# Performance work log

Hardware: AMD Instinct MI355X
Metric: run time of the kernel (lower is better)

## Reference

```python
import jax, jax.numpy as jnp
import numpy as np

B, T, D, H = 128, 512, 256, 256


def setup_inputs() -> dict:
    key = jax.random.key(0)
    k1, k2, k3, k4 = jax.random.split(key, 4)
    x = jax.random.normal(k1, (B, T, D), dtype=jnp.float32)
    x_len = jax.random.randint(k2, (B,), 1, T + 1)  # lengths in [1, T]
    W_ih = jax.random.normal(k3, (4 * H, D), dtype=jnp.float32) * 0.05
    W_hh = jax.random.normal(k4, (4 * H, H), dtype=jnp.float32) * 0.05
    b_ih = jnp.zeros((4 * H,), dtype=jnp.float32)
    # reset_params: bias_hh forget-gate chunk (index 1 of i,f,g,o) set to 1
    b_hh = jnp.zeros((4 * H,), dtype=jnp.float32).at[H:2 * H].set(1.0)
    return {"x": x, "x_len": x_len, "W_ih": W_ih, "W_hh": W_hh,
            "b_ih": b_ih, "b_hh": b_hh}


def reference(x, x_len, W_ih, W_hh, b_ih, b_hh):
    # Dropout is identity in eval mode. The sort/pack/unpack pipeline is
    # mathematically equivalent to running a masked LSTM over the padded
    # batch and zeroing outputs at positions t >= x_len (pad_packed_sequence
    # zero-pads), since output at t < len only depends on steps <= t.
    Bx, Tx, _ = x.shape
    Hh = W_hh.shape[1]
    # Precompute input projections for all timesteps: [B, T, 4H] -> [T, B, 4H]
    xg = jnp.einsum('btd,gd->btg', x, W_ih) + b_ih + b_hh
    xg = jnp.swapaxes(xg, 0, 1)

    def step(carry, xt):
        h, c = carry
        gates = xt + h @ W_hh.T  # [B, 4H]
        i, f, g, o = jnp.split(gates, 4, axis=-1)
        i = jax.nn.sigmoid(i)
        f = jax.nn.sigmoid(f)
        g = jnp.tanh(g)
        o = jax.nn.sigmoid(o)
        c = f * c + i * g
        h = o * jnp.tanh(c)
        return (h, c), h

    h0 = jnp.zeros((Bx, Hh), x.dtype)
    (_, _), hs = jax.lax.scan(step, (h0, h0), xg)  # hs: [T, B, H]
    out = jnp.swapaxes(hs, 0, 1)  # [B, T, H]
    mask = jnp.arange(Tx)[None, :] < x_len[:, None]  # [B, T]
    return jnp.where(mask[..., None], out, jnp.zeros((), x.dtype))
```

## Files before the change

kernel.cpp:

```cpp
#include <hip/hip_runtime.h>
#include <hip/hip_fp16.h>
#include <math.h>

#define BB 128
#define TT 512
#define DD 256
#define HH 256
#define NG 1024

typedef _Float16 h2_t __attribute__((ext_vector_type(2)));
typedef _Float16 f16x8 __attribute__((ext_vector_type(8)));
typedef float f32x4 __attribute__((ext_vector_type(4)));

#if __has_builtin(__builtin_amdgcn_fdot2)
__device__ __forceinline__ float fdot2_(h2_t a, h2_t b, float c) {
    return __builtin_amdgcn_fdot2(a, b, c, false);
}
#else
__device__ __forceinline__ float fdot2_(h2_t a, h2_t b, float c) {
    return c + (float)a.x * (float)b.x + (float)a.y * (float)b.y;
}
#endif

__device__ __forceinline__ float sigmoidf_(float x) {
    return 1.0f / (1.0f + __expf(-x));
}
__device__ __forceinline__ float tanhf_(float x) {
    x = fminf(15.0f, fmaxf(-15.0f, x));
    float e = __expf(2.0f * x);
    return (e - 1.0f) / (e + 1.0f);
}
__device__ __forceinline__ void dot4_(float4& acc, uint4 u, h2_t h) {
    acc.x = fdot2_(__builtin_bit_cast(h2_t, u.x), h, acc.x);
    acc.y = fdot2_(__builtin_bit_cast(h2_t, u.y), h, acc.y);
    acc.z = fdot2_(__builtin_bit_cast(h2_t, u.z), h, acc.z);
    acc.w = fdot2_(__builtin_bit_cast(h2_t, u.w), h, acc.w);
}

#if __has_builtin(__builtin_amdgcn_update_dpp)
__device__ __forceinline__ float pair_sum_(float v) {
    int x = __builtin_bit_cast(int, v);
    int y = __builtin_amdgcn_update_dpp(0, x, 0xB1, 0xF, 0xF, true);
    return v + __builtin_bit_cast(float, y);
}
#else
__device__ __forceinline__ float pair_sum_(float v) {
    return v + __shfl_xor(v, 1, 64);
}
#endif

__global__ void pack2(const float* __restrict__ W_ih, const float* __restrict__ W_hh,
                      const float* __restrict__ b_ih, const float* __restrict__ b_hh,
                      __half* __restrict__ Wg16, __half* __restrict__ Wi16,
                      __half* __restrict__ Wh16, float* __restrict__ bias_p) {
    int idx = blockIdx.x * 256 + threadIdx.x;
    int n = idx >> 8;
    int k = idx & 255;
    int g = (n & 3) * 256 + (n >> 2);
    float wih = W_ih[g * 256 + k];
    float whh = W_hh[g * 256 + k];
    Wg16[n * 256 + k] = __float2half(wih);
    size_t hidx = ((size_t)(k >> 1) * 1024 + n) * 2 + (k & 1);
    Wi16[hidx] = __float2half(wih);
    Wh16[hidx] = __float2half(whh);
    if (idx < 1024) {
        int gg = (idx & 3) * 256 + (idx >> 2);
        bias_p[idx] = b_ih[gg] + b_hh[gg];
    }
}

__global__ __launch_bounds__(256) void cvt_x(const float* __restrict__ X,
                                             __half* __restrict__ X16) {
    size_t i = ((size_t)blockIdx.x * 256 + threadIdx.x) * 8;
    float4 a = *(const float4*)&X[i];
    float4 b = *(const float4*)&X[i + 4];
    f16x8 v;
    v[0] = (_Float16)a.x; v[1] = (_Float16)a.y; v[2] = (_Float16)a.z; v[3] = (_Float16)a.w;
    v[4] = (_Float16)b.x; v[5] = (_Float16)b.y; v[6] = (_Float16)b.z; v[7] = (_Float16)b.w;
    *(f16x8*)&X16[i] = v;
}

__global__ __launch_bounds__(256) void xg_gemm_mfma(const __half* __restrict__ X16,
                                                    const __half* __restrict__ Wg16,
                                                    const float* __restrict__ bias_p,
                                                    __half* __restrict__ xg,
                                                    int t0, int lTc, int tcMask) {
    __shared__ __align__(16) __half st[4][16][72];
    int tid = threadIdx.x;
    int w = tid >> 6, lane = tid & 63;
    int row16 = lane & 15, quad = lane >> 4;
    int m0 = blockIdx.x * 64 + w * 16;
    int n0 = blockIdx.y * 64;

    int mrow = m0 + row16;
    size_t xrow = (size_t)(mrow >> lTc) * 512 + t0 + (mrow & tcMask);
    const __half* aptr = X16 + xrow * 256 + quad * 8;
    f16x8 afrag[8];
#pragma unroll
    for (int kk = 0; kk < 8; ++kk)
        afrag[kk] = *(const f16x8*)(aptr + kk * 32);

#pragma unroll
    for (int cg = 0; cg < 4; ++cg) {
        int n = n0 + cg * 16 + row16;
        const __half* bptr = Wg16 + (size_t)n * 256 + quad * 8;
        f32x4 acc = {0.0f, 0.0f, 0.0f, 0.0f};
#pragma unroll
        for (int kk = 0; kk < 8; ++kk) {
            f16x8 bfrag = *(const f16x8*)(bptr + kk * 32);
            acc = __builtin_amdgcn_mfma_f32_16x16x32_f16(afrag[kk], bfrag, acc, 0, 0, 0);
        }
        float bias = bias_p[n];
#pragma unroll
        for (int r = 0; r < 4; ++r)
            st[w][quad * 4 + r][cg * 16 + row16] = __float2half(acc[r] + bias);
    }
    __syncthreads();
    int ml = lane >> 2, cq = lane & 3;
    int mout = blockIdx.x * 64 + w * 16 + ml;
    const uint4* src = (const uint4*)&st[w][ml][cq * 16];
    uint4 v0 = src[0], v1 = src[1];
    *(uint4*)&xg[(size_t)mout * 1024 + n0 + cq * 16] = v0;
    *(uint4*)&xg[(size_t)mout * 1024 + n0 + cq * 16 + 8] = v1;
}

__global__ __launch_bounds__(512, 2) void lstm_rec4(const __half* __restrict__ xg,
                                                    const __half* __restrict__ Wh16,
                                                    const int* __restrict__ x_len,
                                                    float* __restrict__ out,
                                                    __half* __restrict__ h_state,
                                                    float* __restrict__ c_state,
                                                    int t0, int Tc) {
    __shared__ __align__(16) uint4 lw[9728];
    __shared__ __align__(16) __half hs[2][272];
    int tid = threadIdx.x;
    int c = tid >> 1, kh = tid & 1;
    int b = blockIdx.x;
    int len = x_len[b];
    const uint4* W4 = (const uint4*)Wh16;

    for (int j = tid; j < 9728; j += 512) {
        int i2 = j >> 9, c2 = (j >> 1) & 255, kh2 = j & 1;
        lw[j] = W4[(size_t)(kh2 * 64 + 44 + i2) * 256 + c2];
    }
    const uint4* wp = W4 + (size_t)(kh * 64) * 256 + c;
    uint4 wreg[44];
#pragma unroll
    for (int i = 0; i < 44; ++i) wreg[i] = wp[(size_t)i * 256];

    float cst = 0.0f;
    float hlast = 0.0f;
    if (t0 != 0) cst = c_state[b * 256 + c];
    if (kh == 0)
        hs[0][c + ((c >> 7) << 4)] = (t0 == 0) ? __float2half(0.0f)
                                               : h_state[b * 256 + c];

    const __half* xgb = xg + (size_t)b * Tc * 1024 + 4 * c;
    float* outb = out + ((size_t)b * 512 + t0) * 256 + c;
    const uint4* lwb = lw + tid;
    __syncthreads();

    for (int tt = 0; tt < Tc; ++tt) {
        uint4 s0 = wp[(size_t)63 * 256];
        uint2 xr = *(const uint2*)(xgb + (size_t)tt * 1024);

        const uint4* h4 = (const uint4*)(hs[tt & 1]) + kh * 18;
        float4 acc = {0.0f, 0.0f, 0.0f, 0.0f};
#pragma unroll
        for (int j = 0; j < 11; ++j) {
            uint4 hv = h4[j];
            dot4_(acc, wreg[j * 4 + 0], __builtin_bit_cast(h2_t, hv.x));
            dot4_(acc, wreg[j * 4 + 1], __builtin_bit_cast(h2_t, hv.y));
            dot4_(acc, wreg[j * 4 + 2], __builtin_bit_cast(h2_t, hv.z));
            dot4_(acc, wreg[j * 4 + 3], __builtin_bit_cast(h2_t, hv.w));
        }
#pragma unroll
        for (int j = 11; j < 15; ++j) {
            uint4 hv = h4[j];
            int i0 = (j - 11) * 4;
            dot4_(acc, lwb[(i0 + 0) * 512], __builtin_bit_cast(h2_t, hv.x));
            dot4_(acc, lwb[(i0 + 1) * 512], __builtin_bit_cast(h2_t, hv.y));
            dot4_(acc, lwb[(i0 + 2) * 512], __builtin_bit_cast(h2_t, hv.z));
            dot4_(acc, lwb[(i0 + 3) * 512], __builtin_bit_cast(h2_t, hv.w));
        }
        {
            uint4 hv = h4[15];
            dot4_(acc, lwb[16 * 512], __builtin_bit_cast(h2_t, hv.x));
            dot4_(acc, lwb[17 * 512], __builtin_bit_cast(h2_t, hv.y));
            dot4_(acc, lwb[18 * 512], __builtin_bit_cast(h2_t, hv.z));
            dot4_(acc, s0, __builtin_bit_cast(h2_t, hv.w));
        }
        float gi = pair_sum_(acc.x);
        float gf = pair_sum_(acc.y);
        float gg = pair_sum_(acc.z);
        float go = pair_sum_(acc.w);
        h2_t x01 = __builtin_bit_cast(h2_t, xr.x);
        h2_t x23 = __builtin_bit_cast(h2_t, xr.y);
        gi += (float)x01.x;
        gf += (float)x01.y;
        gg += (float)x23.x;
        go += (float)x23.y;
        float iv = sigmoidf_(gi), fv = sigmoidf_(gf);
        float gv = tanhf_(gg),   ov = sigmoidf_(go);
        cst = fv * cst + iv * gv;
        float h = ov * tanhf_(cst);
        hlast = h;
        if (kh == 0) {
            outb[(size_t)tt * 256] = (t0 + tt < len) ? h : 0.0f;
            hs[(tt & 1) ^ 1][c + ((c >> 7) << 4)] = __float2half(h);
        }
        __syncthreads();
    }
    if (kh == 0) {
        h_state[b * 256 + c] = __float2half(hlast);
        c_state[b * 256 + c] = cst;
    }
}

__global__ __launch_bounds__(1024) void lstm_fused16(const float* __restrict__ X,
                                                     const __half* __restrict__ Wi16,
                                                     const __half* __restrict__ Wh16,
                                                     const float* __restrict__ bias_p,
                                                     const int* __restrict__ x_len,
                                                     float* __restrict__ out) {
    __shared__ __half hs_h[256];
    __shared__ __half xs_h[256];
    __shared__ float4 part[3][256];
    int tid = threadIdx.x;
    int c = tid & 255, kh = tid >> 8;
    int b = blockIdx.x;
    int len = x_len[b];
    float cst = 0.0f;
    float4 bias;
    if (kh == 0) {
        bias = *(const float4*)&bias_p[4 * c];
        hs_h[c] = __float2half(0.0f);
    }
    const uint4* wph = (const uint4*)(Wh16 + (size_t)(kh * 32) * 2048 + 8 * c);
    const uint4* wpi = (const uint4*)(Wi16 + (size_t)(kh * 32) * 2048 + 8 * c);
    float* outb = out + (size_t)b * 512 * 256 + c;
    __syncthreads();

    for (int t = 0; t < TT; ++t) {
        if (tid < 128) {
            float2 xv = *(const float2*)&X[((size_t)b * 512 + t) * 256 + 2 * tid];
            h2_t xh = {(_Float16)xv.x, (_Float16)xv.y};
            ((h2_t*)xs_h)[tid] = xh;
        }
        __syncthreads();
        float4 acc = {0.0f, 0.0f, 0.0f, 0.0f};
#pragma unroll 4
        for (int i = 0; i < 32; ++i) {
            uint4 uh = wph[(size_t)i * 256];
            uint4 ui = wpi[(size_t)i * 256];
            h2_t hv = ((const h2_t*)hs_h)[kh * 32 + i];
            h2_t xv = ((const h2_t*)xs_h)[kh * 32 + i];
            dot4_(acc, uh, hv);
            dot4_(acc, ui, xv);
        }
        if (kh) part[kh - 1][c] = acc;
        __syncthreads();
        if (kh == 0) {
            float4 p0 = part[0][c], p1 = part[1][c], p2 = part[2][c];
            float gi = acc.x + p0.x + p1.x + p2.x + bias.x;
            float gf = acc.y + p0.y + p1.y + p2.y + bias.y;
            float gg = acc.z + p0.z + p1.z + p2.z + bias.z;
            float go = acc.w + p0.w + p1.w + p2.w + bias.w;
            float iv = sigmoidf_(gi), fv = sigmoidf_(gf);
            float gv = tanhf_(gg),   ov = sigmoidf_(go);
            cst = fv * cst + iv * gv;
            float h = ov * tanhf_(cst);
            outb[(size_t)t * 256] = (t < len) ? h : 0.0f;
            hs_h[c] = __float2half(h);
        }
        __syncthreads();
    }
}

extern "C" void kernel_launch(void* const* d_in, const int* in_sizes, int n_in,
                              void* d_out, int out_size, void* d_ws, size_t ws_size,
                              hipStream_t stream) {
    const float* x     = (const float*)d_in[0];
    const int*   x_len = (const int*)d_in[1];
    const float* W_ih  = (const float*)d_in[2];
    const float* W_hh  = (const float*)d_in[3];
    const float* b_ih  = (const float*)d_in[4];
    const float* b_hh  = (const float*)d_in[5];
    float* out = (float*)d_out;

    char* ws = (char*)d_ws;
    __half* Wh16    = (__half*)(ws);
    __half* Wi16    = (__half*)(ws + 0x080000);
    __half* Wg16    = (__half*)(ws + 0x100000);
    float*  bias_p  = (float*)(ws + 0x180000);
    __half* h_state = (__half*)(ws + 0x181000);
    float*  c_state = (float*)(ws + 0x191000);
    __half* x16     = (__half*)(ws + 0x1B1000);
    size_t  o_xg    = 0x1B1000 + (size_t)0x2004000;
    __half* xg      = (__half*)(ws + o_xg);

    int Tc = 0;
    for (int cand = 512; cand >= 16; cand >>= 1)
        if (ws_size >= o_xg + (size_t)cand * 262144) { Tc = cand; break; }

    pack2<<<1024, 256, 0, stream>>>(W_ih, W_hh, b_ih, b_hh,
                                    Wg16, Wi16, Wh16, bias_p);
    if (Tc) {
        cvt_x<<<8192, 256, 0, stream>>>(x, x16);
        int lTc = 31 - __builtin_clz((unsigned)Tc);
        for (int t0 = 0; t0 < TT; t0 += Tc) {
            dim3 g(2 * Tc, 16);
            xg_gemm_mfma<<<g, 256, 0, stream>>>(x16, Wg16, bias_p, xg,
                                                t0, lTc, Tc - 1);
            lstm_rec4<<<BB, 512, 0, stream>>>(xg, Wh16, x_len, out,
                                              h_state, c_state, t0, Tc);
        }
    } else {
        lstm_fused16<<<BB, 1024, 0, stream>>>(x, Wi16, Wh16, bias_p, x_len, out);
    }
}
```

Measured before the change: 1.238 ms.

## Hold recurrent weights in AccVGPRs instead of LDS and per-step global loads

Moves most of the per-thread W_hh slice (48 of 64 uint4) into accumulation registers via inline asm constraints and reads them with v_accvgpr_read each step. It drops the large LDS weight buffer and the per-timestep global load of the last weight row, keeping 16 uint4 in ordinary VGPRs. The aim is to remove LDS bandwidth and global-load latency from the serial recurrence loop. In exchange it adds an extra accvgpr-read instruction per weight dword and carries register-allocation and spill risk under 512-thread launch bounds.

```diff
diff --git a/kernel.cpp b/kernel.cpp
--- a/kernel.cpp
+++ b/kernel.cpp
@@ -35,6 +35,12 @@
     acc.y = fdot2_(__builtin_bit_cast(h2_t, u.y), h, acc.y);
     acc.z = fdot2_(__builtin_bit_cast(h2_t, u.z), h, acc.z);
     acc.w = fdot2_(__builtin_bit_cast(h2_t, u.w), h, acc.w);
+}
+
+__device__ __forceinline__ uint ar_(const uint& a, int dep) {
+    uint v;
+    asm("v_accvgpr_read_b32 %0, %1" : "=v"(v) : "a"(a), "v"(dep));
+    return v;
 }
 
 #if __has_builtin(__builtin_amdgcn_update_dpp)
@@ -131,7 +137,6 @@
                                                     __half* __restrict__ h_state,
                                                     float* __restrict__ c_state,
                                                     int t0, int Tc) {
-    __shared__ __align__(16) uint4 lw[9728];
     __shared__ __align__(16) __half hs[2][272];
     int tid = threadIdx.x;
     int c = tid >> 1, kh = tid & 1;
@@ -139,14 +144,17 @@
     int len = x_len[b];
     const uint4* W4 = (const uint4*)Wh16;
 
-    for (int j = tid; j < 9728; j += 512) {
-        int i2 = j >> 9, c2 = (j >> 1) & 255, kh2 = j & 1;
-        lw[j] = W4[(size_t)(kh2 * 64 + 44 + i2) * 256 + c2];
-    }
     const uint4* wp = W4 + (size_t)(kh * 64) * 256 + c;
-    uint4 wreg[44];
-#pragma unroll
-    for (int i = 0; i < 44; ++i) wreg[i] = wp[(size_t)i * 256];
+    uint4 wreg[16];
+#pragma unroll
+    for (int i = 0; i < 16; ++i) wreg[i] = wp[(size_t)i * 256];
+    uint4 wa4[48];
+#pragma unroll
+    for (int i = 0; i < 48; ++i) wa4[i] = wp[(size_t)(16 + i) * 256];
+#pragma unroll
+    for (int i = 0; i < 48; ++i)
+        asm volatile("" : "+a"(wa4[i].x), "+a"(wa4[i].y),
+                          "+a"(wa4[i].z), "+a"(wa4[i].w));
 
     float cst = 0.0f;
     float hlast = 0.0f;
@@ -157,39 +165,39 @@
 
     const __half* xgb = xg + (size_t)b * Tc * 1024 + 4 * c;
     float* outb = out + ((size_t)b * 512 + t0) * 256 + c;
-    const uint4* lwb = lw + tid;
     __syncthreads();
 
     for (int tt = 0; tt < Tc; ++tt) {
-        uint4 s0 = wp[(size_t)63 * 256];
         uint2 xr = *(const uint2*)(xgb + (size_t)tt * 1024);
 
         const uint4* h4 = (const uint4*)(hs[tt & 1]) + kh * 18;
         float4 acc = {0.0f, 0.0f, 0.0f, 0.0f};
 #pragma unroll
-        for (int j = 0; j < 11; ++j) {
+        for (int j = 0; j < 4; ++j) {
             uint4 hv = h4[j];
             dot4_(acc, wreg[j * 4 + 0], __builtin_bit_cast(h2_t, hv.x));
             dot4_(acc, wreg[j * 4 + 1], __builtin_bit_cast(h2_t, hv.y));
             dot4_(acc, wreg[j * 4 + 2], __builtin_bit_cast(h2_t, hv.z));
             dot4_(acc, wreg[j * 4 + 3], __builtin_bit_cast(h2_t, hv.w));
         }
-#pragma unroll
-        for (int j = 11; j < 15; ++j) {
+#define DOT4A(ai, hx)                                                          \
+        {                                                                      \
+            h2_t hh = __builtin_bit_cast(h2_t, hx);                            \
+            acc.x = fdot2_(__builtin_bit_cast(h2_t, ar_(wa4[ai].x, tt)), hh, acc.x); \
+            acc.y = fdot2_(__builtin_bit_cast(h2_t, ar_(wa4[ai].y, tt)), hh, acc.y); \
+            acc.z = fdot2_(__builtin_bit_cast(h2_t, ar_(wa4[ai].z, tt)), hh, acc.z); \
+            acc.w = fdot2_(__builtin_bit_cast(h2_t, ar_(wa4[ai].w, tt)), hh, acc.w); \
+        }
+#pragma unroll
+        for (int j = 4; j < 16; ++j) {
             uint4 hv = h4[j];
-            int i0 = (j - 11) * 4;
-            dot4_(acc, lwb[(i0 + 0) * 512], __builtin_bit_cast(h2_t, hv.x));
-            dot4_(acc, lwb[(i0 + 1) * 512], __builtin_bit_cast(h2_t, hv.y));
-            dot4_(acc, lwb[(i0 + 2) * 512], __builtin_bit_cast(h2_t, hv.z));
-            dot4_(acc, lwb[(i0 + 3) * 512], __builtin_bit_cast(h2_t, hv.w));
-        }
-        {
-            uint4 hv = h4[15];
-            dot4_(acc, lwb[16 * 512], __builtin_bit_cast(h2_t, hv.x));
-            dot4_(acc, lwb[17 * 512], __builtin_bit_cast(h2_t, hv.y));
-            dot4_(acc, lwb[18 * 512], __builtin_bit_cast(h2_t, hv.z));
-            dot4_(acc, s0, __builtin_bit_cast(h2_t, hv.w));
-        }
+            int a0 = (j - 4) * 4;
+            DOT4A(a0 + 0, hv.x);
+            DOT4A(a0 + 1, hv.y);
+            DOT4A(a0 + 2, hv.z);
+            DOT4A(a0 + 3, hv.w);
+        }
+#undef DOT4A
         float gi = pair_sum_(acc.x);
         float gf = pair_sum_(acc.y);
         float gg = pair_sum_(acc.z);
```

After: 4.169 ms. 3.37x slower.
